# Kernel optimization log

Measured on AMD Instinct MI355X. Metric: run time of the kernel, lower is better.

The kernel has to match this reference:

```python
import jax, jax.numpy as jnp
import numpy as np

B, L, D = 4, 4096, 256


def setup_inputs() -> dict:
    key = jax.random.key(0)
    k_x, k_q, k_k, k_v, k_w, k_b = jax.random.split(key, 6)
    s = 1.0 / np.sqrt(D)
    return {
        "x": jax.random.normal(k_x, (B, L, D), dtype=jnp.float32),
        "Wq": jax.random.normal(k_q, (D, D), dtype=jnp.float32) * s,   # nn.Linear weight (out,in)
        "Wk": jax.random.normal(k_k, (D, D), dtype=jnp.float32) * s,
        "Wv": jax.random.normal(k_v, (D, D), dtype=jnp.float32) * s,
        "w_mlp": jax.random.normal(k_w, (D,), dtype=jnp.float32) * s,  # Linear(D,1) weight
        "b_mlp": jnp.zeros((), dtype=jnp.float32),                     # Linear(D,1) bias
    }


def reference(x, Wq, Wk, Wv, w_mlp, b_mlp):
    # Projections (nn.Linear: y = x @ W.T, no bias)
    Q = jnp.einsum("bld,ed->ble", x, Wq)
    K = jnp.einsum("bld,ed->ble", x, Wk)
    V = jnp.einsum("bld,ed->ble", x, Wv)
    # score[b,i,j] = relu((Q[b,i]-K[b,j]) @ w_mlp + b_mlp)
    # decomposed: (Q-K)@w = Q@w - K@w  (exact same math, no (B,L,L,D) tensor)
    q_s = Q @ w_mlp  # (B,L)
    k_s = K @ w_mlp  # (B,L)
    scores = jax.nn.relu(q_s[:, :, None] - k_s[:, None, :] + b_mlp)  # (B,L,L)
    attn = jax.nn.softmax(scores, axis=-1)  # softmax over key axis j
    # out[b,i,d] = sum_j attn[b,i,j] * V[b,j,d]
    out = jnp.einsum("bij,bjd->bid", attn, V)
    return out  # dropout p=0.0 is identity
```

## Files before the change

### kernel.cpp

```cpp
#include <hip/hip_runtime.h>
#include <math.h>

#define BB 4
#define LL 4096
#define DD 256
#define NROWS (BB*LL)
#define CHUNK 32
#define NC (LL/CHUNK)
#define NB 8192

typedef __bf16 bf16x8 __attribute__((ext_vector_type(8)));
typedef __bf16 bf16x4 __attribute__((ext_vector_type(4)));
typedef float floatx4 __attribute__((ext_vector_type(4)));

__global__ void k_uvec(const float* __restrict__ Wq, const float* __restrict__ Wk,
                       const float* __restrict__ w, float* __restrict__ u) {
    __shared__ float wl[16];
    int d = threadIdx.x;
    int e0 = blockIdx.x * 16;
    if (d < 16) wl[d] = w[e0 + d];
    __syncthreads();
    float aq = 0.f, ak = 0.f;
    #pragma unroll
    for (int j = 0; j < 16; ++j) {
        float we = wl[j];
        aq = fmaf(Wq[(size_t)(e0 + j)*DD + d], we, aq);
        ak = fmaf(Wk[(size_t)(e0 + j)*DD + d], we, ak);
    }
    atomicAdd(&u[d], aq);
    atomicAdd(&u[DD + d], ak);
}

__global__ void k_split(const float* __restrict__ x, const float* __restrict__ Wv,
                        const float* __restrict__ u, const float* __restrict__ bmlp,
                        __bf16* __restrict__ xh, __bf16* __restrict__ xl,
                        __bf16* __restrict__ Wh, __bf16* __restrict__ Wl,
                        float* __restrict__ a, float* __restrict__ c) {
    int lane = threadIdx.x & 63;
    if (blockIdx.x < NROWS/4) {
        int row = blockIdx.x * 4 + (threadIdx.x >> 6);
        float4 xv = ((const float4*)(x + (size_t)row * DD))[lane];
        __bf16 h0 = (__bf16)xv.x, h1 = (__bf16)xv.y, h2 = (__bf16)xv.z, h3 = (__bf16)xv.w;
        __bf16 l0 = (__bf16)(xv.x - (float)h0), l1 = (__bf16)(xv.y - (float)h1);
        __bf16 l2 = (__bf16)(xv.z - (float)h2), l3 = (__bf16)(xv.w - (float)h3);
        bf16x4 hv = {h0, h1, h2, h3};
        bf16x4 lv = {l0, l1, l2, l3};
        *(bf16x4*)(xh + (size_t)row * DD + lane*4) = hv;
        *(bf16x4*)(xl + (size_t)row * DD + lane*4) = lv;
        float4 uq = ((const float4*)u)[lane];
        float4 uk = ((const float4*)(u + DD))[lane];
        float sq = xv.x*uq.x + xv.y*uq.y + xv.z*uq.z + xv.w*uq.w;
        float sk = xv.x*uk.x + xv.y*uk.y + xv.z*uk.z + xv.w*uk.w;
        #pragma unroll
        for (int off = 32; off > 0; off >>= 1) {
            sq += __shfl_down(sq, off);
            sk += __shfl_down(sk, off);
        }
        if (lane == 0) {
            a[row] = sq + bmlp[0];
            c[row] = sk;
        }
    } else {
        int wrow = (blockIdx.x - NROWS/4) * 4 + (threadIdx.x >> 6);
        float4 wv = ((const float4*)(Wv + (size_t)wrow * DD))[lane];
        __bf16 h0 = (__bf16)wv.x, h1 = (__bf16)wv.y, h2 = (__bf16)wv.z, h3 = (__bf16)wv.w;
        __bf16 l0 = (__bf16)(wv.x - (float)h0), l1 = (__bf16)(wv.y - (float)h1);
        __bf16 l2 = (__bf16)(wv.z - (float)h2), l3 = (__bf16)(wv.w - (float)h3);
        bf16x4 hv = {h0, h1, h2, h3};
        bf16x4 lv = {l0, l1, l2, l3};
        *(bf16x4*)(Wh + (size_t)wrow * DD + lane*4) = hv;
        *(bf16x4*)(Wl + (size_t)wrow * DD + lane*4) = lv;
    }
}

__global__ void __launch_bounds__(256) k_gemm_mfma(
        const __bf16* __restrict__ xh, const __bf16* __restrict__ xl,
        const __bf16* __restrict__ Wh, const __bf16* __restrict__ Wl,
        float* __restrict__ V) {
    __shared__ __bf16 Ah[32*40];
    __shared__ __bf16 Al[32*40];
    __shared__ __bf16 Bh[256*40];
    __shared__ __bf16 Bl[256*40];
    const int tid = threadIdx.x;
    const int wave = tid >> 6, lane = tid & 63;
    const int rowBase = blockIdx.x * 32;
    const int quad = lane >> 4, l16 = lane & 15;

    floatx4 acc[2][4];
    #pragma unroll
    for (int rt = 0; rt < 2; ++rt)
        #pragma unroll
        for (int ct = 0; ct < 4; ++ct)
            acc[rt][ct] = (floatx4){0.f, 0.f, 0.f, 0.f};

    for (int k0 = 0; k0 < DD; k0 += 32) {
        __syncthreads();
        {
            int row = tid >> 3, kq = (tid & 7) * 4;
            *(bf16x4*)&Ah[row*40 + kq] = *(const bf16x4*)(xh + (size_t)(rowBase + row)*DD + k0 + kq);
            *(bf16x4*)&Al[row*40 + kq] = *(const bf16x4*)(xl + (size_t)(rowBase + row)*DD + k0 + kq);
        }
        {
            int n = tid;
            #pragma unroll
            for (int p = 0; p < 4; ++p) {
                *(bf16x8*)&Bh[n*40 + p*8] = *(const bf16x8*)(Wh + (size_t)n*DD + k0 + p*8);
                *(bf16x8*)&Bl[n*40 + p*8] = *(const bf16x8*)(Wl + (size_t)n*DD + k0 + p*8);
            }
        }
        __syncthreads();
        bf16x8 ah[2], al[2], bh[4], bl[4];
        #pragma unroll
        for (int rt = 0; rt < 2; ++rt) {
            int m = rt*16 + l16;
            ah[rt] = *(bf16x8*)&Ah[m*40 + quad*8];
            al[rt] = *(bf16x8*)&Al[m*40 + quad*8];
        }
        #pragma unroll
        for (int ct = 0; ct < 4; ++ct) {
            int n = wave*64 + ct*16 + l16;
            bh[ct] = *(bf16x8*)&Bh[n*40 + quad*8];
            bl[ct] = *(bf16x8*)&Bl[n*40 + quad*8];
        }
        #pragma unroll
        for (int rt = 0; rt < 2; ++rt)
            #pragma unroll
            for (int ct = 0; ct < 4; ++ct) {
                acc[rt][ct] = __builtin_amdgcn_mfma_f32_16x16x32_bf16(ah[rt], bh[ct], acc[rt][ct], 0, 0, 0);
                acc[rt][ct] = __builtin_amdgcn_mfma_f32_16x16x32_bf16(ah[rt], bl[ct], acc[rt][ct], 0, 0, 0);
                acc[rt][ct] = __builtin_amdgcn_mfma_f32_16x16x32_bf16(al[rt], bh[ct], acc[rt][ct], 0, 0, 0);
            }
    }
    #pragma unroll
    for (int rt = 0; rt < 2; ++rt)
        #pragma unroll
        for (int ct = 0; ct < 4; ++ct)
            #pragma unroll
            for (int i = 0; i < 4; ++i) {
                int row = rowBase + rt*16 + quad*4 + i;
                int col = wave*64 + ct*16 + l16;
                V[(size_t)row*DD + col] = acc[rt][ct][i];
            }
}

__global__ void __launch_bounds__(1024) k_sortish(const float* __restrict__ c,
        int* __restrict__ binstart_g, int* __restrict__ perm,
        float* __restrict__ c_sorted, float* __restrict__ e_sorted,
        float* __restrict__ SE, float* __restrict__ hdr) {
    __shared__ float cl[LL];
    __shared__ int   hist[NB];
    __shared__ float esl[LL];
    __shared__ float scrf[64];
    int b = blockIdx.x, tid = threadIdx.x;
    int wave = tid >> 6, lane = tid & 63;
    int* scri = (int*)scrf;

    float4 cv = ((const float4*)(c + (size_t)b*LL))[tid];
    ((float4*)cl)[tid] = cv;
    float cw[4] = {cv.x, cv.y, cv.z, cv.w};
    float mn = fminf(fminf(cw[0],cw[1]), fminf(cw[2],cw[3]));
    float mx = fmaxf(fmaxf(cw[0],cw[1]), fmaxf(cw[2],cw[3]));
    #pragma unroll
    for (int off = 32; off > 0; off >>= 1) {
        mn = fminf(mn, __shfl_down(mn, off));
        mx = fmaxf(mx, __shfl_down(mx, off));
    }
    if (lane == 0) { scrf[wave] = mn; scrf[32 + wave] = mx; }
    __syncthreads();
    if (wave == 0) {
        float m = (lane < 16) ? scrf[lane]      :  3.4e38f;
        float M = (lane < 16) ? scrf[32 + lane] : -3.4e38f;
        #pragma unroll
        for (int off = 32; off > 0; off >>= 1) {
            m = fminf(m, __shfl_down(m, off));
            M = fmaxf(M, __shfl_down(M, off));
        }
        if (lane == 0) { scrf[0] = m; scrf[1] = M; }
    }
    __syncthreads();
    float cmin = scrf[0], cmax = scrf[1];
    float scale = (float)NB / fmaxf(cmax - cmin, 1e-20f);
    __syncthreads();

    ((int4*)hist)[tid] = make_int4(0,0,0,0);
    ((int4*)hist)[tid + 1024] = make_int4(0,0,0,0);
    __syncthreads();

    int bins[4];
    #pragma unroll
    for (int u = 0; u < 4; ++u) {
        int bi = (int)((cw[u] - cmin) * scale);
        bi = bi < 0 ? 0 : (bi > NB-1 ? NB-1 : bi);
        bins[u] = bi;
        atomicAdd(&hist[bi], 1);
    }
    __syncthreads();

    int loc[8]; int base = 0;
    #pragma unroll
    for (int j = 0; j < 8; ++j) { loc[j] = base; base += hist[tid*8 + j]; }
    int incl = base;
    #pragma unroll
    for (int off = 1; off < 64; off <<= 1) {
        int t = __shfl_up(incl, off);
        if (lane >= off) incl += t;
    }
    if (lane == 63) scri[wave] = incl;
    __syncthreads();
    if (wave == 0) {
        int v = (lane < 16) ? scri[lane] : 0;
        int s = v;
        #pragma unroll
        for (int off = 1; off < 16; off <<= 1) {
            int t = __shfl_up(s, off);
            if (lane >= off) s += t;
        }
        if (lane < 16) scri[lane] = s - v;
    }
    __syncthreads();
    int thread_excl = (incl - base) + scri[wave];
    __syncthreads();
    #pragma unroll
    for (int j = 0; j < 8; ++j) {
        int bs = thread_excl + loc[j];
        binstart_g[(size_t)b*(NB+2) + tid*8 + j] = bs;
        hist[tid*8 + j] = bs;
    }
    if (tid == 0) {
        binstart_g[(size_t)b*(NB+2) + NB]     = LL;
        binstart_g[(size_t)b*(NB+2) + NB + 1] = LL;
        hdr[b*2 + 0] = cmin;
        hdr[b*2 + 1] = scale;
    }
    __syncthreads();

    #pragma unroll
    for (int u = 0; u < 4; ++u) {
        int i = tid*4 + u;
        int r = atomicAdd(&hist[bins[u]], 1);
        float e = expf(cmin - cw[u]);
        perm[(size_t)b*LL + r] = i;
        c_sorted[(size_t)b*LL + r] = cw[u];
        e_sorted[(size_t)b*LL + r] = e;
        esl[r] = e;
    }
    __syncthreads();

    float le[4]; float s0 = 0.f;
    #pragma unroll
    for (int u = 0; u < 4; ++u) { le[u] = s0; s0 += esl[tid*4 + u]; }
    float fincl = s0;
    #pragma unroll
    for (int off = 1; off < 64; off <<= 1) {
        float t = __shfl_up(fincl, off);
        if (lane >= off) fincl += t;
    }
    if (lane == 63) scrf[wave] = fincl;
    __syncthreads();
    if (wave == 0) {
        float v = (lane < 16) ? scrf[lane] : 0.f;
        float s = v;
        #pragma unroll
        for (int off = 1; off < 16; off <<= 1) {
            float t = __shfl_up(s, off);
            if (lane >= off) s += t;
        }
        if (lane < 16) scrf[lane] = s - v;
    }
    __syncthreads();
    float texcl = (fincl - s0) + scrf[wave];
    #pragma unroll
    for (int u = 0; u < 4; ++u)
        SE[(size_t)b*(LL+1) + tid*4 + u] = texcl + le[u];
    if (tid == 1023) SE[(size_t)b*(LL+1) + LL] = texcl + s0;
}

__global__ void k_scan(const float* __restrict__ V, const int* __restrict__ perm,
        const float* __restrict__ e_sorted,
        float* __restrict__ Pl, float* __restrict__ Pel,
        float* __restrict__ Tp, float* __restrict__ Te) {
    int b = blockIdx.y, q = blockIdx.x;
    int d = threadIdx.x;
    __shared__ int pj[CHUNK];
    __shared__ float pe[CHUNK];
    if (d < CHUNK) {
        pj[d] = perm[(size_t)b*LL + q*CHUNK + d];
        pe[d] = e_sorted[(size_t)b*LL + q*CHUNK + d];
    }
    __syncthreads();
    float vr[CHUNK];
    #pragma unroll
    for (int r = 0; r < CHUNK; ++r)
        vr[r] = V[((size_t)b*LL + pj[r]) * DD + d];
    float acc = 0.f, acce = 0.f;
    size_t kb = (size_t)b*LL + (size_t)q*CHUNK;
    #pragma unroll
    for (int r = 0; r < CHUNK; ++r) {
        size_t o = (kb + r) * DD + d;
        Pl[o]  = acc;
        Pel[o] = acce;
        acc += vr[r];
        acce = fmaf(pe[r], vr[r], acce);
    }
    size_t to = ((size_t)b*NC + q) * DD + d;
    Tp[to] = acc;
    Te[to] = acce;
}

__global__ void k_base(const float* __restrict__ Tp, const float* __restrict__ Te,
        float* __restrict__ baseP, float* __restrict__ basePe) {
    int b = blockIdx.x, d = threadIdx.x;
    float acc = 0.f, acce = 0.f;
    #pragma unroll 16
    for (int q = 0; q < NC; ++q) {
        size_t o = ((size_t)b*(NC+1) + q) * DD + d;
        baseP[o] = acc; basePe[o] = acce;
        size_t ti = ((size_t)b*NC + q) * DD + d;
        acc += Tp[ti]; acce += Te[ti];
    }
    size_t o = ((size_t)b*(NC+1) + NC) * DD + d;
    baseP[o] = acc; basePe[o] = acce;
}

__global__ void k_out(const float* __restrict__ a, const float* __restrict__ hdr,
                      const int* __restrict__ binstart,
                      const float* __restrict__ c_sorted, const float* __restrict__ e_sorted,
                      const int* __restrict__ perm, const float* __restrict__ V,
                      const float* __restrict__ SE,
                      const float* __restrict__ Pl, const float* __restrict__ Pel,
                      const float* __restrict__ baseP, const float* __restrict__ basePe,
                      float* __restrict__ out) {
    int row = blockIdx.x * 4 + (threadIdx.x >> 6);
    int lane = threadIdx.x & 63;
    int b = row >> 12;
    float ai = a[row];
    float cmin = hdr[b*2 + 0], scale = hdr[b*2 + 1];
    float t = (ai - cmin) * scale;
    int ib = t < 0.f ? 0 : (t >= (float)NB ? NB : (int)t);
    int k    = binstart[(size_t)b*(NB+2) + ib];
    int kend = binstart[(size_t)b*(NB+2) + ib + 1];
    float alpha = expf(cmin - ai);
    float Z = fmaf(alpha, (float)(LL - k), SE[(size_t)b*(LL+1) + k]);
    size_t db = (size_t)lane * 4;
    size_t totoff = ((size_t)b * (NC+1) + NC) * DD + db;
    float4 ptot  = *(const float4*)(baseP  + totoff);
    float4 pk, pek;
    if (k < LL) {
        int q = k >> 5;
        size_t po = ((size_t)b * LL + k) * DD + db;
        size_t bo = ((size_t)b * (NC+1) + q) * DD + db;
        float4 pl = *(const float4*)(Pl    + po);
        float4 bp = *(const float4*)(baseP + bo);
        float4 pe = *(const float4*)(Pel    + po);
        float4 be = *(const float4*)(basePe + bo);
        pk.x = pl.x + bp.x; pk.y = pl.y + bp.y; pk.z = pl.z + bp.z; pk.w = pl.w + bp.w;
        pek.x = pe.x + be.x; pek.y = pe.y + be.y; pek.z = pe.z + be.z; pek.w = pe.w + be.w;
    } else {
        pk = ptot;
        float4 pt = *(const float4*)(basePe + totoff);
        pek = pt;
    }
    float4 num;
    num.x = fmaf(alpha, ptot.x - pk.x, pek.x);
    num.y = fmaf(alpha, ptot.y - pk.y, pek.y);
    num.z = fmaf(alpha, ptot.z - pk.z, pek.z);
    num.w = fmaf(alpha, ptot.w - pk.w, pek.w);
    for (int r = k; r < kend; ++r) {
        float cr = c_sorted[(size_t)b*LL + r];
        if (cr < ai) {
            float w = e_sorted[(size_t)b*LL + r] - alpha;
            int j = perm[(size_t)b*LL + r];
            float4 v = *(const float4*)(V + ((size_t)b*LL + j) * DD + db);
            num.x = fmaf(w, v.x, num.x);
            num.y = fmaf(w, v.y, num.y);
            num.z = fmaf(w, v.z, num.z);
            num.w = fmaf(w, v.w, num.w);
            Z += w;
        }
    }
    float invZ = 1.f / Z;
    float4 o;
    o.x = num.x * invZ; o.y = num.y * invZ; o.z = num.z * invZ; o.w = num.w * invZ;
    *(float4*)(out + (size_t)row * DD + db) = o;
}

extern "C" void kernel_launch(void* const* d_in, const int* in_sizes, int n_in,
                              void* d_out, int out_size, void* d_ws, size_t ws_size,
                              hipStream_t stream) {
    const float* x  = (const float*)d_in[0];
    const float* Wq = (const float*)d_in[1];
    const float* Wk = (const float*)d_in[2];
    const float* Wv = (const float*)d_in[3];
    const float* wm = (const float*)d_in[4];
    const float* bm = (const float*)d_in[5];
    float* out = (float*)d_out;
    float* ws = (float*)d_ws;

    size_t off = 0;
    auto alloc = [&](size_t n) {
        float* p = ws + off;
        off += (n + 255) & ~(size_t)255;
        return p;
    };
    float* u        = alloc(2*DD);
    float* a        = alloc(NROWS);
    float* c        = alloc(NROWS);
    float* c_sorted = alloc(NROWS);
    float* e_sorted = alloc(NROWS);
    float* SE       = alloc((size_t)BB*(LL+1));
    int*   perm     = (int*)alloc(NROWS);
    int*   binstart = (int*)alloc((size_t)BB*(NB+2));
    float* hdr      = alloc(2*BB);
    float* V        = alloc((size_t)NROWS*DD);
    float* Pl       = alloc((size_t)NROWS*DD);
    float* Pel      = alloc((size_t)NROWS*DD);
    float* Tp       = alloc((size_t)BB*NC*DD);
    float* Te       = alloc((size_t)BB*NC*DD);
    float* baseP    = alloc((size_t)BB*(NC+1)*DD);
    float* basePe   = alloc((size_t)BB*(NC+1)*DD);
    __bf16* xh      = (__bf16*)alloc((size_t)NROWS*DD/2);
    __bf16* xl      = (__bf16*)alloc((size_t)NROWS*DD/2);
    __bf16* Wh      = (__bf16*)alloc((size_t)DD*DD/2);
    __bf16* Wl      = (__bf16*)alloc((size_t)DD*DD/2);

    hipMemsetAsync(u, 0, 2*DD*sizeof(float), stream);
    hipLaunchKernelGGL(k_uvec, dim3(16), dim3(DD), 0, stream, Wq, Wk, wm, u);
    hipLaunchKernelGGL(k_split, dim3(NROWS/4 + DD/4), dim3(256), 0, stream,
                       x, Wv, u, bm, xh, xl, Wh, Wl, a, c);
    hipLaunchKernelGGL(k_gemm_mfma, dim3(NROWS/32), dim3(256), 0, stream,
                       xh, xl, Wh, Wl, V);
    hipLaunchKernelGGL(k_sortish, dim3(BB), dim3(1024), 0, stream,
                       c, binstart, perm, c_sorted, e_sorted, SE, hdr);
    hipLaunchKernelGGL(k_scan, dim3(NC, BB), dim3(DD), 0, stream, V, perm, e_sorted, Pl, Pel, Tp, Te);
    hipLaunchKernelGGL(k_base, dim3(BB), dim3(DD), 0, stream, Tp, Te, baseP, basePe);
    hipLaunchKernelGGL(k_out, dim3(NROWS/4), dim3(256), 0, stream,
                       a, hdr, binstart, c_sorted, e_sorted, perm, V,
                       SE, Pl, Pel, baseP, basePe, out);
}
```

Measured before the change: 146.2 us.

## Fuse x bf16 split and score dots into GEMM, parallelize base prefix

The split kernel is removed: the GEMM now reads fp32 x directly, splits it into bf16 hi/lo in shared memory and accumulates the q/k score dot products alongside, reducing them at the end. This drops the xh/xl round trip through global memory and one launch. The Wv hi/lo split moves into the u-vector kernel. B tiles are now read straight from global/L2 per wave instead of being staged in LDS. The k_base kernel becomes one block per chunk, each summing all prior chunk totals, trading serial latency for redundant reads.

```diff
diff --git a/kernel.cpp b/kernel.cpp
--- a/kernel.cpp
+++ b/kernel.cpp
@@ -13,8 +13,10 @@
 typedef __bf16 bf16x4 __attribute__((ext_vector_type(4)));
 typedef float floatx4 __attribute__((ext_vector_type(4)));
 
-__global__ void k_uvec(const float* __restrict__ Wq, const float* __restrict__ Wk,
-                       const float* __restrict__ w, float* __restrict__ u) {
+__global__ void k_prep(const float* __restrict__ Wq, const float* __restrict__ Wk,
+                       const float* __restrict__ Wv, const float* __restrict__ w,
+                       float* __restrict__ u,
+                       __bf16* __restrict__ Wh, __bf16* __restrict__ Wl) {
     __shared__ float wl[16];
     int d = threadIdx.x;
     int e0 = blockIdx.x * 16;
@@ -26,65 +28,31 @@
         float we = wl[j];
         aq = fmaf(Wq[(size_t)(e0 + j)*DD + d], we, aq);
         ak = fmaf(Wk[(size_t)(e0 + j)*DD + d], we, ak);
+        float wv = Wv[(size_t)(e0 + j)*DD + d];
+        __bf16 h = (__bf16)wv;
+        Wh[(size_t)(e0 + j)*DD + d] = h;
+        Wl[(size_t)(e0 + j)*DD + d] = (__bf16)(wv - (float)h);
     }
     atomicAdd(&u[d], aq);
     atomicAdd(&u[DD + d], ak);
 }
 
-__global__ void k_split(const float* __restrict__ x, const float* __restrict__ Wv,
-                        const float* __restrict__ u, const float* __restrict__ bmlp,
-                        __bf16* __restrict__ xh, __bf16* __restrict__ xl,
-                        __bf16* __restrict__ Wh, __bf16* __restrict__ Wl,
-                        float* __restrict__ a, float* __restrict__ c) {
-    int lane = threadIdx.x & 63;
-    if (blockIdx.x < NROWS/4) {
-        int row = blockIdx.x * 4 + (threadIdx.x >> 6);
-        float4 xv = ((const float4*)(x + (size_t)row * DD))[lane];
-        __bf16 h0 = (__bf16)xv.x, h1 = (__bf16)xv.y, h2 = (__bf16)xv.z, h3 = (__bf16)xv.w;
-        __bf16 l0 = (__bf16)(xv.x - (float)h0), l1 = (__bf16)(xv.y - (float)h1);
-        __bf16 l2 = (__bf16)(xv.z - (float)h2), l3 = (__bf16)(xv.w - (float)h3);
-        bf16x4 hv = {h0, h1, h2, h3};
-        bf16x4 lv = {l0, l1, l2, l3};
-        *(bf16x4*)(xh + (size_t)row * DD + lane*4) = hv;
-        *(bf16x4*)(xl + (size_t)row * DD + lane*4) = lv;
-        float4 uq = ((const float4*)u)[lane];
-        float4 uk = ((const float4*)(u + DD))[lane];
-        float sq = xv.x*uq.x + xv.y*uq.y + xv.z*uq.z + xv.w*uq.w;
-        float sk = xv.x*uk.x + xv.y*uk.y + xv.z*uk.z + xv.w*uk.w;
-        #pragma unroll
-        for (int off = 32; off > 0; off >>= 1) {
-            sq += __shfl_down(sq, off);
-            sk += __shfl_down(sk, off);
-        }
-        if (lane == 0) {
-            a[row] = sq + bmlp[0];
-            c[row] = sk;
-        }
-    } else {
-        int wrow = (blockIdx.x - NROWS/4) * 4 + (threadIdx.x >> 6);
-        float4 wv = ((const float4*)(Wv + (size_t)wrow * DD))[lane];
-        __bf16 h0 = (__bf16)wv.x, h1 = (__bf16)wv.y, h2 = (__bf16)wv.z, h3 = (__bf16)wv.w;
-        __bf16 l0 = (__bf16)(wv.x - (float)h0), l1 = (__bf16)(wv.y - (float)h1);
-        __bf16 l2 = (__bf16)(wv.z - (float)h2), l3 = (__bf16)(wv.w - (float)h3);
-        bf16x4 hv = {h0, h1, h2, h3};
-        bf16x4 lv = {l0, l1, l2, l3};
-        *(bf16x4*)(Wh + (size_t)wrow * DD + lane*4) = hv;
-        *(bf16x4*)(Wl + (size_t)wrow * DD + lane*4) = lv;
-    }
-}
-
 __global__ void __launch_bounds__(256) k_gemm_mfma(
-        const __bf16* __restrict__ xh, const __bf16* __restrict__ xl,
+        const float* __restrict__ x,
         const __bf16* __restrict__ Wh, const __bf16* __restrict__ Wl,
-        float* __restrict__ V) {
+        const float* __restrict__ u, const float* __restrict__ bmlp,
+        float* __restrict__ V, float* __restrict__ a, float* __restrict__ c) {
     __shared__ __bf16 Ah[32*40];
     __shared__ __bf16 Al[32*40];
-    __shared__ __bf16 Bh[256*40];
-    __shared__ __bf16 Bl[256*40];
+    __shared__ float4 ul[128];
+    __shared__ float pros[512];
     const int tid = threadIdx.x;
     const int wave = tid >> 6, lane = tid & 63;
     const int rowBase = blockIdx.x * 32;
     const int quad = lane >> 4, l16 = lane & 15;
+    const int srow = tid >> 3, skq = (tid & 7) * 4;
+
+    if (tid < 128) ul[tid] = ((const float4*)u)[tid];
 
     floatx4 acc[2][4];
     #pragma unroll
@@ -92,24 +60,23 @@
         #pragma unroll
         for (int ct = 0; ct < 4; ++ct)
             acc[rt][ct] = (floatx4){0.f, 0.f, 0.f, 0.f};
+    float aq = 0.f, ak = 0.f;
 
     for (int k0 = 0; k0 < DD; k0 += 32) {
         __syncthreads();
-        {
-            int row = tid >> 3, kq = (tid & 7) * 4;
-            *(bf16x4*)&Ah[row*40 + kq] = *(const bf16x4*)(xh + (size_t)(rowBase + row)*DD + k0 + kq);
-            *(bf16x4*)&Al[row*40 + kq] = *(const bf16x4*)(xl + (size_t)(rowBase + row)*DD + k0 + kq);
-        }
-        {
-            int n = tid;
-            #pragma unroll
-            for (int p = 0; p < 4; ++p) {
-                *(bf16x8*)&Bh[n*40 + p*8] = *(const bf16x8*)(Wh + (size_t)n*DD + k0 + p*8);
-                *(bf16x8*)&Bl[n*40 + p*8] = *(const bf16x8*)(Wl + (size_t)n*DD + k0 + p*8);
-            }
-        }
+        float4 xv = *(const float4*)(x + (size_t)(rowBase + srow)*DD + k0 + skq);
+        __bf16 h0 = (__bf16)xv.x, h1 = (__bf16)xv.y, h2 = (__bf16)xv.z, h3 = (__bf16)xv.w;
+        bf16x4 hv = {h0, h1, h2, h3};
+        bf16x4 lv = {(__bf16)(xv.x - (float)h0), (__bf16)(xv.y - (float)h1),
+                     (__bf16)(xv.z - (float)h2), (__bf16)(xv.w - (float)h3)};
+        *(bf16x4*)&Ah[srow*40 + skq] = hv;
+        *(bf16x4*)&Al[srow*40 + skq] = lv;
+        float4 q4 = ul[(k0 >> 2) + (tid & 7)];
+        float4 k4 = ul[64 + (k0 >> 2) + (tid & 7)];
+        aq = fmaf(xv.x, q4.x, fmaf(xv.y, q4.y, fmaf(xv.z, q4.z, fmaf(xv.w, q4.w, aq))));
+        ak = fmaf(xv.x, k4.x, fmaf(xv.y, k4.y, fmaf(xv.z, k4.z, fmaf(xv.w, k4.w, ak))));
         __syncthreads();
-        bf16x8 ah[2], al[2], bh[4], bl[4];
+        bf16x8 ah[2], al[2];
         #pragma unroll
         for (int rt = 0; rt < 2; ++rt) {
             int m = rt*16 + l16;
@@ -119,17 +86,15 @@
         #pragma unroll
         for (int ct = 0; ct < 4; ++ct) {
             int n = wave*64 + ct*16 + l16;
-            bh[ct] = *(bf16x8*)&Bh[n*40 + quad*8];
-            bl[ct] = *(bf16x8*)&Bl[n*40 + quad*8];
-        }
-        #pragma unroll
-        for (int rt = 0; rt < 2; ++rt)
+            bf16x8 bh = *(const bf16x8*)(Wh + (size_t)n*DD + k0 + quad*8);
+            bf16x8 bl = *(const bf16x8*)(Wl + (size_t)n*DD + k0 + quad*8);
             #pragma unroll
-            for (int ct = 0; ct < 4; ++ct) {
-                acc[rt][ct] = __builtin_amdgcn_mfma_f32_16x16x32_bf16(ah[rt], bh[ct], acc[rt][ct], 0, 0, 0);
-                acc[rt][ct] = __builtin_amdgcn_mfma_f32_16x16x32_bf16(ah[rt], bl[ct], acc[rt][ct], 0, 0, 0);
-                acc[rt][ct] = __builtin_amdgcn_mfma_f32_16x16x32_bf16(al[rt], bh[ct], acc[rt][ct], 0, 0, 0);
+            for (int rt = 0; rt < 2; ++rt) {
+                acc[rt][ct] = __builtin_amdgcn_mfma_f32_16x16x32_bf16(ah[rt], bh, acc[rt][ct], 0, 0, 0);
+                acc[rt][ct] = __builtin_amdgcn_mfma_f32_16x16x32_bf16(ah[rt], bl, acc[rt][ct], 0, 0, 0);
+                acc[rt][ct] = __builtin_amdgcn_mfma_f32_16x16x32_bf16(al[rt], bh, acc[rt][ct], 0, 0, 0);
             }
+        }
     }
     #pragma unroll
     for (int rt = 0; rt < 2; ++rt)
@@ -141,6 +106,20 @@
                 int col = wave*64 + ct*16 + l16;
                 V[(size_t)row*DD + col] = acc[rt][ct][i];
             }
+    __syncthreads();
+    pros[tid] = aq;
+    pros[256 + tid] = ak;
+    __syncthreads();
+    if (tid < 32) {
+        float sa = 0.f, sc = 0.f;
+        #pragma unroll
+        for (int j = 0; j < 8; ++j) {
+            sa += pros[tid*8 + j];
+            sc += pros[256 + tid*8 + j];
+        }
+        a[rowBase + tid] = sa + bmlp[0];
+        c[rowBase + tid] = sc;
+    }
 }
 
 __global__ void __launch_bounds__(1024) k_sortish(const float* __restrict__ c,
@@ -309,16 +288,14 @@
 
 __global__ void k_base(const float* __restrict__ Tp, const float* __restrict__ Te,
         float* __restrict__ baseP, float* __restrict__ basePe) {
-    int b = blockIdx.x, d = threadIdx.x;
+    int q = blockIdx.x, b = blockIdx.y, d = threadIdx.x;
     float acc = 0.f, acce = 0.f;
-    #pragma unroll 16
-    for (int q = 0; q < NC; ++q) {
-        size_t o = ((size_t)b*(NC+1) + q) * DD + d;
-        baseP[o] = acc; basePe[o] = acce;
-        size_t ti = ((size_t)b*NC + q) * DD + d;
+    #pragma unroll 8
+    for (int i = 0; i < q; ++i) {
+        size_t ti = ((size_t)b*NC + i) * DD + d;
         acc += Tp[ti]; acce += Te[ti];
     }
-    size_t o = ((size_t)b*(NC+1) + NC) * DD + d;
+    size_t o = ((size_t)b*(NC+1) + q) * DD + d;
     baseP[o] = acc; basePe[o] = acce;
 }
 
@@ -418,21 +395,17 @@
     float* Te       = alloc((size_t)BB*NC*DD);
     float* baseP    = alloc((size_t)BB*(NC+1)*DD);
     float* basePe   = alloc((size_t)BB*(NC+1)*DD);
-    __bf16* xh      = (__bf16*)alloc((size_t)NROWS*DD/2);
-    __bf16* xl      = (__bf16*)alloc((size_t)NROWS*DD/2);
     __bf16* Wh      = (__bf16*)alloc((size_t)DD*DD/2);
     __bf16* Wl      = (__bf16*)alloc((size_t)DD*DD/2);
 
     hipMemsetAsync(u, 0, 2*DD*sizeof(float), stream);
-    hipLaunchKernelGGL(k_uvec, dim3(16), dim3(DD), 0, stream, Wq, Wk, wm, u);
-    hipLaunchKernelGGL(k_split, dim3(NROWS/4 + DD/4), dim3(256), 0, stream,
-                       x, Wv, u, bm, xh, xl, Wh, Wl, a, c);
+    hipLaunchKernelGGL(k_prep, dim3(16), dim3(DD), 0, stream, Wq, Wk, Wv, wm, u, Wh, Wl);
     hipLaunchKernelGGL(k_gemm_mfma, dim3(NROWS/32), dim3(256), 0, stream,
-                       xh, xl, Wh, Wl, V);
+                       x, Wh, Wl, u, bm, V, a, c);
     hipLaunchKernelGGL(k_sortish, dim3(BB), dim3(1024), 0, stream,
                        c, binstart, perm, c_sorted, e_sorted, SE, hdr);
     hipLaunchKernelGGL(k_scan, dim3(NC, BB), dim3(DD), 0, stream, V, perm, e_sorted, Pl, Pel, Tp, Te);
-    hipLaunchKernelGGL(k_base, dim3(BB), dim3(DD), 0, stream, Tp, Te, baseP, basePe);
+    hipLaunchKernelGGL(k_base, dim3(NC+1, BB), dim3(DD), 0, stream, Tp, Te, baseP, basePe);
     hipLaunchKernelGGL(k_out, dim3(NROWS/4), dim3(256), 0, stream,
                        a, hdr, binstart, c_sorted, e_sorted, perm, V,
                        SE, Pl, Pel, baseP, basePe, out);
```

After: 137.5 us. 6.0% less time.
